# Kernel tuning notes

Hardware: AMD Instinct MI355X
Metric: run time of the kernel (lower is better)

Reference implementation:

```python
import jax, jax.numpy as jnp
import numpy as np

N = 1024       # nodes
D1 = 64        # hidden_dim_1
D2 = 64        # hidden_dim_2
E = 16384      # edges
P = 8192       # query pairs
MAXX = 100     # max node label -> Embedding(MAXX+1, D1)
EPS = 1e-5     # LayerNorm eps (no affine)


def _ln(t):
    m = jnp.mean(t, axis=-1, keepdims=True)
    v = jnp.mean((t - m) ** 2, axis=-1, keepdims=True)
    return (t - m) / jnp.sqrt(v + EPS)


def setup_inputs() -> dict:
    key = jax.random.key(0)
    ks = jax.random.split(key, 12)
    s = 0.1
    x = jax.random.randint(ks[0], (N,), 0, MAXX + 1)
    ei = jax.random.randint(ks[1], (2, E), 0, N)
    pos = jax.random.randint(ks[2], (P, 2), 0, N)
    emb = jax.random.normal(ks[3], (MAXX + 1, D1)) * s
    sage_Wl = jax.random.normal(ks[4], (2, D1, D1)) * s   # lin_l weight (aggr path, has bias)
    sage_bl = jnp.zeros((2, D1))
    sage_Wr = jax.random.normal(ks[5], (2, D1, D1)) * s   # lin_r weight (root path, no bias)
    h_W = jax.random.normal(ks[6], (D1 + 1, D2)) * s
    h_b = jnp.zeros((D2,))
    g_W = jax.random.normal(ks[7], (D1 + 1 + 2 * D2, D2)) * s
    g_b = jnp.zeros((D2,))
    lin_W = jax.random.normal(ks[8], (D2, 1)) * s
    lin_b = jnp.zeros((1,))
    return {"x": x, "ei": ei, "pos": pos, "emb": emb,
            "sage_Wl": sage_Wl, "sage_bl": sage_bl, "sage_Wr": sage_Wr,
            "h_W": h_W, "h_b": h_b, "g_W": g_W, "g_b": g_b,
            "lin_W": lin_W, "lin_b": lin_b}


def reference(x, ei, pos, emb, sage_Wl, sage_bl, sage_Wr, h_W, h_b, g_W, g_b, lin_W, lin_b):
    n = N
    src, dst = ei[0], ei[1]
    h = emb[x]                                            # (n, D1)
    # SAGEConv x2: mean-aggregate src->dst, lin_l(aggr)+bias + lin_r(root); then LN (no affine, no relu)
    deg = jax.ops.segment_sum(jnp.ones((E,), h.dtype), dst, num_segments=n)
    deg = jnp.maximum(deg, 1.0)[:, None]
    for i in range(2):
        aggr = jax.ops.segment_sum(h[src], dst, num_segments=n) / deg
        h = _ln(aggr @ sage_Wl[i] + sage_bl[i] + h @ sage_Wr[i])
    # pairwise outer product features: (n, n, D1)
    A = h[:, None, :] * h[None, :, :]
    eim = jnp.zeros((n * n,), h.dtype).at[src * n + dst].set(1.0).reshape(n, n, 1)
    A = jnp.concatenate([A, eim], axis=-1)                # (n, n, D1+1)
    # mataggr: B = h_1(A); row/col sums; D = cat(A, vec_p, vec_q); g_1(D)
    B = jax.nn.relu(_ln(A @ h_W + h_b))                   # (n, n, D2)
    vec_p = jnp.sum(B, axis=1, keepdims=True)             # (n, 1, D2)
    vec_q = jnp.sum(B, axis=0, keepdims=True)             # (1, n, D2)
    Dm = jnp.concatenate([A,
                          jnp.broadcast_to(vec_p, (n, n, D2)),
                          jnp.broadcast_to(vec_q, (n, n, D2))], axis=-1)
    G = jax.nn.relu(_ln(Dm @ g_W + g_b))                  # (n, n, D2)
    # symmetrize and gather query pairs
    S = (G * jnp.transpose(G, (1, 0, 2))).reshape(n * n, D2)
    sel = S[pos[:, 0] * n + pos[:, 1]]                    # (P, D2)
    return sel @ lin_W + lin_b                            # (P, 1)
```

## Files before the change

kernel.cpp:

```cpp
#include <hip/hip_runtime.h>
#include <hip/hip_bf16.h>

#define NN 1024
#define DD 64
#define EE 16384
#define PP 8192
#define EPSF 1e-5f
#define SWP (DD + 8)

typedef __hip_bfloat16 bf16;
typedef __attribute__((ext_vector_type(8))) short short8;
typedef __attribute__((ext_vector_type(4))) float f32x4;

static __device__ __forceinline__ float dec1(const void* src, int i, int fl) {
    if (fl) return ((const float*)src)[i];
    return __bfloat162float(((const bf16*)src)[i]);
}
static __device__ __forceinline__ unsigned short f2bf_u(float f) {
    bf16 h = __float2bfloat16(f);
    return *reinterpret_cast<unsigned short*>(&h);
}
static __device__ __forceinline__ float bfu2f(unsigned short u) {
    return __uint_as_float(((unsigned int)u) << 16);
}
static __device__ __forceinline__ int probe_fl(const void* emb) {
    int lane = threadIdx.x & 63;
    unsigned short raw = ((const unsigned short*)emb)[lane];
    float v = __uint_as_float(((unsigned int)raw) << 16);
    return (__ballot(!(fabsf(v) <= 1e3f)) != 0ull) ? 1 : 0;
}

__global__ __launch_bounds__(1024) void k_prep(
        const void* __restrict__ emb, const void* __restrict__ sWl,
        const void* __restrict__ sbl, const void* __restrict__ sWr,
        const void* __restrict__ hW, const void* __restrict__ hb,
        const void* __restrict__ gW, const void* __restrict__ gb,
        const void* __restrict__ lW, const void* __restrict__ lb,
        const int* __restrict__ x, const int* __restrict__ ei,
        float* __restrict__ Wlf, float* __restrict__ blf, float* __restrict__ Wrf,
        float* __restrict__ WfT, float* __restrict__ hbw,
        float* __restrict__ gWf, float* __restrict__ linf,
        float* __restrict__ h0,
        unsigned int* __restrict__ eim, unsigned int* __restrict__ eimT,
        int* __restrict__ rowptr, int* __restrict__ csrc) {
    __shared__ int sdeg[NN];
    __shared__ int stmp[1024];
    const int b = blockIdx.x, tid = threadIdx.x;
    const int fl = probe_fl(emb);

    if (b < 97) {
        const int vb = b * 4 + (tid >> 8);
        const int vt = tid & 255;
        if (vb < 256) {
            int z = vb * 256 + vt;
            if (z < 32768) eim[z] = 0u;
            else           eimT[z - 32768] = 0u;
        }
        if (vb < 32) { int i = vb * 256 + vt; Wlf[i] = dec1(sWl, i, fl); }
        else if (vb == 32) { if (vt < 128) blf[vt] = dec1(sbl, vt, fl); }
        else if (vb < 65) { int i = (vb - 33) * 256 + vt; Wrf[i] = dec1(sWr, i, fl); }
        else if (vb < 82) {
            int i = (vb - 65) * 256 + vt;
            if (i < 4096) { int n = i >> 6, k = i & 63; WfT[n * DD + k] = dec1(hW, k * DD + n, fl); }
            else if (i < 4160) hbw[i - 4096] = dec1(hb, i - 4096, fl);
            else if (i < 4224) hbw[64 + (i - 4160)] = dec1(hW, 64 * DD + (i - 4160), fl);
        } else if (vb < 131) {
            int i = (vb - 82) * 256 + vt;
            if (i < 193 * DD) gWf[i] = dec1(gW, i, fl);
            else if (i < 194 * DD) gWf[i] = dec1(gb, i - 193 * DD, fl);
        } else if (vb == 131) {
            if (vt < DD) linf[vt] = dec1(lW, vt, fl);
            else if (vt == DD) linf[DD] = dec1(lb, 0, fl);
        } else if (vb < 388) {
            int i = (vb - 132) * 256 + vt;
            int node = i >> 6, f = i & 63;
            h0[i] = dec1(emb, x[node] * DD + f, fl);
        }
    } else {
        sdeg[tid] = 0;
        __syncthreads();
        for (int base = 0; base < EE; base += 8192) {
            int d8[8];
#pragma unroll
            for (int u = 0; u < 8; ++u) d8[u] = ei[EE + base + u * 1024 + tid];
#pragma unroll
            for (int u = 0; u < 8; ++u) atomicAdd(&sdeg[d8[u]], 1);
        }
        __syncthreads();
        int v = sdeg[tid];
        stmp[tid] = v;
        __syncthreads();
        for (int off = 1; off < 1024; off <<= 1) {
            int a = (tid >= off) ? stmp[tid - off] : 0;
            __syncthreads();
            stmp[tid] += a;
            __syncthreads();
        }
        int excl = stmp[tid] - v;
        rowptr[tid] = excl;
        sdeg[tid] = excl;
        if (tid == 1023) rowptr[NN] = stmp[1023];
        __syncthreads();
        for (int base = 0; base < EE; base += 8192) {
            int d8[8], s8[8];
#pragma unroll
            for (int u = 0; u < 8; ++u) {
                d8[u] = ei[EE + base + u * 1024 + tid];
                s8[u] = ei[base + u * 1024 + tid];
            }
#pragma unroll
            for (int u = 0; u < 8; ++u) {
                int c = atomicAdd(&sdeg[d8[u]], 1);
                csrc[c] = s8[u];
            }
        }
    }
}

static __device__ __forceinline__ void sage_body(
        char* smem, int node, int lane, int wave,
        const int* __restrict__ rowptr, const int* __restrict__ csrc,
        const float* __restrict__ hin,
        const float* __restrict__ Wl, const float* __restrict__ bl,
        const float* __restrict__ Wr,
        float* __restrict__ hout, unsigned short* __restrict__ hbf) {
    float* sa = (float*)smem + wave * 2 * DD;
    float* sh = sa + DD;
    int r0 = rowptr[node], r1 = rowptr[node + 1];
    float s = 0.f;
    for (int r = r0; r < r1; ++r) s += hin[csrc[r] * DD + lane];
    sa[lane] = s / (float)max(r1 - r0, 1);
    sh[lane] = hin[node * DD + lane];
    float o = bl[lane];
    for (int k = 0; k < DD; ++k)
        o += sa[k] * Wl[k * DD + lane] + sh[k] * Wr[k * DD + lane];
    float m = o;
    for (int off = 32; off; off >>= 1) m += __shfl_xor(m, off);
    m *= (1.f / DD);
    float d0 = o - m;
    float v = d0 * d0;
    for (int off = 32; off; off >>= 1) v += __shfl_xor(v, off);
    v *= (1.f / DD);
    float r = d0 * rsqrtf(v + EPSF);
    hout[node * DD + lane] = r;
    if (hbf) hbf[node * DD + lane] = f2bf_u(r);
}

__global__ __launch_bounds__(256) void k_sage0(
        const int* __restrict__ ei,
        const int* __restrict__ rowptr, const int* __restrict__ csrc,
        const float* __restrict__ h0,
        const float* __restrict__ Wlf, const float* __restrict__ blf,
        const float* __restrict__ Wrf,
        float* __restrict__ h1,
        unsigned int* __restrict__ eim, unsigned int* __restrict__ eimT) {
    __shared__ __align__(16) char smem[4 * 2 * DD * 4];
    const int b = blockIdx.x, tid = threadIdx.x;
    const int lane = tid & 63, wave = tid >> 6;
    if (tid < 64) {
        int e = b * 64 + tid;
        int s = ei[e], d = ei[EE + e];
        unsigned int idx = (unsigned int)(s * NN + d);
        atomicOr(&eim[idx >> 5], 1u << (idx & 31));
        unsigned int idxT = (unsigned int)(d * NN + s);
        atomicOr(&eimT[idxT >> 5], 1u << (idxT & 31));
    }
    sage_body(smem, b * 4 + wave, lane, wave, rowptr, csrc, h0, Wlf, blf, Wrf,
              h1, (unsigned short*)nullptr);
}

__global__ __launch_bounds__(256) void k_sage1(
        const int* __restrict__ rowptr, const int* __restrict__ csrc,
        const float* __restrict__ h1,
        const float* __restrict__ Wlf, const float* __restrict__ blf,
        const float* __restrict__ Wrf,
        float* __restrict__ h2, unsigned short* __restrict__ hbf) {
    __shared__ __align__(16) char smem[4 * 2 * DD * 4];
    const int b = blockIdx.x, tid = threadIdx.x;
    const int lane = tid & 63, wave = tid >> 6;
    sage_body(smem, b * 4 + wave, lane, wave, rowptr, csrc, h1,
              Wlf + DD * DD, blf + DD, Wrf + DD * DD, h2, hbf);
}

__global__ __launch_bounds__(256) void k_bstage(
        const float* __restrict__ h2, const unsigned short* __restrict__ hbf,
        const float* __restrict__ WfT, const float* __restrict__ hbw,
        const unsigned int* __restrict__ eim, const unsigned int* __restrict__ eimT,
        const float* __restrict__ gWf,
        float* __restrict__ ppb, float* __restrict__ qqb) {
    __shared__ __align__(16) unsigned short sW[DD * SWP];
    __shared__ __align__(16) float red[4 * 128];
    const int b = blockIdx.x, tid = threadIdx.x;
    const int lane = tid & 63, wave = tid >> 6;
    const int l15 = lane & 15, quad = lane >> 4;

    {
        int m = tid >> 2;
        int k0 = (tid & 3) * 16;
        const float* hi = h2 + b * DD;
        const float* wr = WfT + m * DD;
        unsigned short tmp[16];
#pragma unroll
        for (int u = 0; u < 16; ++u) tmp[u] = f2bf_u(hi[k0 + u] * wr[k0 + u]);
        *(short8*)(sW + m * SWP + k0) = *(short8*)tmp;
        *(short8*)(sW + m * SWP + k0 + 8) = *(short8*)(tmp + 8);
    }
    __syncthreads();

    short8 Af[4][2];
#pragma unroll
    for (int mt = 0; mt < 4; ++mt)
#pragma unroll
        for (int kt = 0; kt < 2; ++kt)
            Af[mt][kt] = *(const short8*)(sW + (mt * 16 + l15) * SWP + kt * 32 + quad * 8);

    float hb0[4][4], hww[4][4];
#pragma unroll
    for (int mt = 0; mt < 4; ++mt) {
        f32x4 a = *(const f32x4*)(hbw + mt * 16 + quad * 4);
        f32x4 wv = *(const f32x4*)(hbw + 64 + mt * 16 + quad * 4);
#pragma unroll
        for (int r = 0; r < 4; ++r) { hb0[mt][r] = a[r]; hww[mt][r] = wv[r]; }
    }

    float accf[4][4], accb[4][4];
#pragma unroll
    for (int mt = 0; mt < 4; ++mt)
#pragma unroll
        for (int r = 0; r < 4; ++r) { accf[mt][r] = 0.f; accb[mt][r] = 0.f; }

    int g = wave;
    short8 B0 = *(const short8*)(hbf + (g * 16 + l15) * DD + quad * 8);
    short8 B1 = *(const short8*)(hbf + (g * 16 + l15) * DD + 32 + quad * 8);

    for (int it = 0; it < 16; ++it, g += 4) {
        short8 cB0 = B0, cB1 = B1;
        if (it < 15) {
            int gn = g + 4;
            B0 = *(const short8*)(hbf + (gn * 16 + l15) * DD + quad * 8);
            B1 = *(const short8*)(hbf + (gn * 16 + l15) * DD + 32 + quad * 8);
        }
        unsigned int base = (unsigned int)(b * NN + g * 16);
        unsigned int sf = (eim[base >> 5] >> (base & 31)) & 0xFFFFu;
        unsigned int sb = (eimT[base >> 5] >> (base & 31)) & 0xFFFFu;

        f32x4 C[4];
#pragma unroll
        for (int mt = 0; mt < 4; ++mt)
            C[mt] = (f32x4){hb0[mt][0], hb0[mt][1], hb0[mt][2], hb0[mt][3]};
#pragma unroll
        for (int mt = 0; mt < 4; ++mt)
            C[mt] = __builtin_amdgcn_mfma_f32_16x16x32_bf16(Af[mt][0], cB0, C[mt], 0, 0, 0);
#pragma unroll
        for (int mt = 0; mt < 4; ++mt)
            C[mt] = __builtin_amdgcn_mfma_f32_16x16x32_bf16(Af[mt][1], cB1, C[mt], 0, 0, 0);

        float ef = (float)((sf >> l15) & 1u);
        float s1 = 0.f, s2 = 0.f;
#pragma unroll
        for (int mt = 0; mt < 4; ++mt)
#pragma unroll
            for (int r = 0; r < 4; ++r) {
                float v = C[mt][r] + ef * hww[mt][r];
                C[mt][r] = v;
                s1 += v;
                s2 += v * v;
            }
        s1 += __shfl_xor(s1, 16); s1 += __shfl_xor(s1, 32);
        s2 += __shfl_xor(s2, 16); s2 += __shfl_xor(s2, 32);
        float mean = s1 * (1.f / DD);
        float var = fmaxf(s2 * (1.f / DD) - mean * mean, 0.f);
        float rs = rsqrtf(var + EPSF);
        float mrs = mean * rs;

        if (sf == sb) {
#pragma unroll
            for (int mt = 0; mt < 4; ++mt)
#pragma unroll
                for (int r = 0; r < 4; ++r) {
                    float u = fmaxf(C[mt][r] * rs - mrs, 0.f);
                    accf[mt][r] += u;
                    accb[mt][r] += u;
                }
        } else {
#pragma unroll
            for (int mt = 0; mt < 4; ++mt)
#pragma unroll
                for (int r = 0; r < 4; ++r)
                    accf[mt][r] += fmaxf(C[mt][r] * rs - mrs, 0.f);
            float de = (float)((sb >> l15) & 1u) - ef;
            float t1 = 0.f, t2 = 0.f;
#pragma unroll
            for (int mt = 0; mt < 4; ++mt)
#pragma unroll
                for (int r = 0; r < 4; ++r) {
                    float v = C[mt][r] + de * hww[mt][r];
                    C[mt][r] = v;
                    t1 += v;
                    t2 += v * v;
                }
            t1 += __shfl_xor(t1, 16); t1 += __shfl_xor(t1, 32);
            t2 += __shfl_xor(t2, 16); t2 += __shfl_xor(t2, 32);
            float mean2 = t1 * (1.f / DD);
            float var2 = fmaxf(t2 * (1.f / DD) - mean2 * mean2, 0.f);
            float rs2 = rsqrtf(var2 + EPSF);
            float mrs2 = mean2 * rs2;
#pragma unroll
            for (int mt = 0; mt < 4; ++mt)
#pragma unroll
                for (int r = 0; r < 4; ++r)
                    accb[mt][r] += fmaxf(C[mt][r] * rs2 - mrs2, 0.f);
        }
    }

#pragma unroll
    for (int step = 1; step < 16; step <<= 1)
#pragma unroll
        for (int mt = 0; mt < 4; ++mt)
#pragma unroll
            for (int r = 0; r < 4; ++r) {
                accf[mt][r] += __shfl_xor(accf[mt][r], step);
                accb[mt][r] += __shfl_xor(accb[mt][r], step);
            }
    if (l15 == 0) {
#pragma unroll
        for (int mt = 0; mt < 4; ++mt)
#pragma unroll
            for (int r = 0; r < 4; ++r) {
                int m = mt * 16 + quad * 4 + r;
                red[wave * 128 + m] = accf[mt][r];
                red[wave * 128 + DD + m] = accb[mt][r];
            }
    }
    __syncthreads();
    if (tid < 128) {
        float sum = red[tid] + red[128 + tid] + red[256 + tid] + red[384 + tid];
        red[tid] = sum;
    }
    __syncthreads();
    if (wave < 2) {
        const float* sv = red + wave * DD;
        int row0 = wave ? 129 : 65;
        float o = 0.f;
        for (int k = 0; k < DD; ++k) o += sv[k] * gWf[(row0 + k) * DD + lane];
        (wave ? qqb : ppb)[b * DD + lane] = o;
    }
}

__global__ __launch_bounds__(256) void k_final(
        const void* __restrict__ emb,
        const int* __restrict__ pos, const unsigned short* __restrict__ hbf,
        const float* __restrict__ gWf, const unsigned int* __restrict__ eim,
        const float* __restrict__ ppb, const float* __restrict__ qqb,
        const float* __restrict__ linf, void* __restrict__ outv) {
    __shared__ __align__(16) unsigned short sgW[DD * SWP];
    const int b = blockIdx.x, tid = threadIdx.x;
    const int lane = tid & 63, wave = tid >> 6;
    const int l15 = lane & 15, quad = lane >> 4;
    const int fl = probe_fl(emb);

    {
        int m = tid >> 2;
        int k0 = (tid & 3) * 16;
        unsigned short tmp[16];
#pragma unroll
        for (int u = 0; u < 16; ++u) tmp[u] = f2bf_u(gWf[(k0 + u) * DD + m]);
        *(short8*)(sgW + m * SWP + k0) = *(short8*)tmp;
        *(short8*)(sgW + m * SWP + k0 + 8) = *(short8*)(tmp + 8);
    }

    int pp_ = b * 64 + wave * 16 + l15;
    int a = pos[2 * pp_], bb = pos[2 * pp_ + 1];
    short8 ha0 = *(const short8*)(hbf + a * DD + quad * 8);
    short8 hb0v = *(const short8*)(hbf + bb * DD + quad * 8);
    short8 ha1 = *(const short8*)(hbf + a * DD + 32 + quad * 8);
    short8 hb1v = *(const short8*)(hbf + bb * DD + 32 + quad * 8);
    short8 B0, B1;
#pragma unroll
    for (int j = 0; j < 8; ++j) {
        B0[j] = (short)f2bf_u(bfu2f((unsigned short)ha0[j]) * bfu2f((unsigned short)hb0v[j]));
        B1[j] = (short)f2bf_u(bfu2f((unsigned short)ha1[j]) * bfu2f((unsigned short)hb1v[j]));
    }
    __syncthreads();

    f32x4 C[4];
#pragma unroll
    for (int mt = 0; mt < 4; ++mt) C[mt] = (f32x4){0.f, 0.f, 0.f, 0.f};
#pragma unroll
    for (int mt = 0; mt < 4; ++mt) {
        short8 A0 = *(const short8*)(sgW + (mt * 16 + l15) * SWP + quad * 8);
        C[mt] = __builtin_amdgcn_mfma_f32_16x16x32_bf16(A0, B0, C[mt], 0, 0, 0);
    }
#pragma unroll
    for (int mt = 0; mt < 4; ++mt) {
        short8 A1 = *(const short8*)(sgW + (mt * 16 + l15) * SWP + 32 + quad * 8);
        C[mt] = __builtin_amdgcn_mfma_f32_16x16x32_bf16(A1, B1, C[mt], 0, 0, 0);
    }

    unsigned int iab = (unsigned int)(a * NN + bb), iba = (unsigned int)(bb * NN + a);
    float eab = (float)((eim[iab >> 5] >> (iab & 31)) & 1u);
    float eba = (float)((eim[iba >> 5] >> (iba & 31)) & 1u);

    float u1[4][4], u2[4][4];
    float s1 = 0.f, s12 = 0.f, s2 = 0.f, s22 = 0.f;
#pragma unroll
    for (int mt = 0; mt < 4; ++mt) {
        int m0 = mt * 16 + quad * 4;
        f32x4 w64v = *(const f32x4*)(gWf + 64 * DD + m0);
        f32x4 gbv  = *(const f32x4*)(gWf + 193 * DD + m0);
        f32x4 ppa  = *(const f32x4*)(ppb + a * DD + m0);
        f32x4 qqb_ = *(const f32x4*)(qqb + bb * DD + m0);
        f32x4 ppb_ = *(const f32x4*)(ppb + bb * DD + m0);
        f32x4 qqa  = *(const f32x4*)(qqb + a * DD + m0);
#pragma unroll
        for (int r = 0; r < 4; ++r) {
            float v1 = C[mt][r] + eab * w64v[r] + ppa[r] + qqb_[r] + gbv[r];
            float v2 = C[mt][r] + eba * w64v[r] + ppb_[r] + qqa[r] + gbv[r];
            u1[mt][r] = v1; u2[mt][r] = v2;
            s1 += v1; s12 += v1 * v1;
            s2 += v2; s22 += v2 * v2;
        }
    }
    s1 += __shfl_xor(s1, 16);  s1 += __shfl_xor(s1, 32);
    s12 += __shfl_xor(s12, 16); s12 += __shfl_xor(s12, 32);
    s2 += __shfl_xor(s2, 16);  s2 += __shfl_xor(s2, 32);
    s22 += __shfl_xor(s22, 16); s22 += __shfl_xor(s22, 32);
    float mean1 = s1 * (1.f / DD);
    float rs1 = rsqrtf(fmaxf(s12 * (1.f / DD) - mean1 * mean1, 0.f) + EPSF);
    float mrs1 = mean1 * rs1;
    float mean2 = s2 * (1.f / DD);
    float rs2 = rsqrtf(fmaxf(s22 * (1.f / DD) - mean2 * mean2, 0.f) + EPSF);
    float mrs2 = mean2 * rs2;

    float r = 0.f;
#pragma unroll
    for (int mt = 0; mt < 4; ++mt) {
        f32x4 lw = *(const f32x4*)(linf + mt * 16 + quad * 4);
#pragma unroll
        for (int rr = 0; rr < 4; ++rr) {
            float g1 = fmaxf(u1[mt][rr] * rs1 - mrs1, 0.f);
            float g2 = fmaxf(u2[mt][rr] * rs2 - mrs2, 0.f);
            r += g1 * g2 * lw[rr];
        }
    }
    r += __shfl_xor(r, 16); r += __shfl_xor(r, 32);
    if (quad == 0) {
        float res = r + linf[DD];
        if (fl) ((float*)outv)[pp_] = res;
        else    ((bf16*)outv)[pp_] = __float2bfloat16(res);
    }
}

extern "C" void kernel_launch(void* const* d_in, const int* in_sizes, int n_in,
                              void* d_out, int out_size, void* d_ws, size_t ws_size,
                              hipStream_t stream) {
    const int* x   = (const int*)d_in[0];
    const int* ei  = (const int*)d_in[1];
    const int* pos = (const int*)d_in[2];
    const void* emb = d_in[3];

    char* w = (char*)d_ws;
    auto alloc = [&](size_t bytes) {
        void* q = (void*)w;
        w += (bytes + 255) & ~(size_t)255;
        return q;
    };
    unsigned int* eim  = (unsigned int*)alloc(NN * NN / 8);
    unsigned int* eimT = (unsigned int*)alloc(NN * NN / 8);
    float* h0   = (float*)alloc(NN * DD * 4);
    float* h1   = (float*)alloc(NN * DD * 4);
    float* h2   = (float*)alloc(NN * DD * 4);
    unsigned short* hbf = (unsigned short*)alloc(NN * DD * 2);
    float* Wlf  = (float*)alloc(2 * DD * DD * 4);
    float* blf  = (float*)alloc(2 * DD * 4);
    float* Wrf  = (float*)alloc(2 * DD * DD * 4);
    float* WfT  = (float*)alloc(DD * DD * 4);
    float* hbw  = (float*)alloc(128 * 4);
    float* gWf  = (float*)alloc(194 * DD * 4);
    float* linf = (float*)alloc(65 * 4);
    float* ppb  = (float*)alloc(NN * DD * 4);
    float* qqb  = (float*)alloc(NN * DD * 4);
    int* rowptr = (int*)alloc((NN + 1) * 4);
    int* csrc   = (int*)alloc(EE * 4);

    k_prep<<<98, 1024, 0, stream>>>(emb, d_in[4], d_in[5], d_in[6], d_in[7], d_in[8],
                                    d_in[9], d_in[10], d_in[11], d_in[12],
                                    x, ei, Wlf, blf, Wrf, WfT, hbw, gWf, linf,
                                    h0, eim, eimT, rowptr, csrc);
    k_sage0<<<256, 256, 0, stream>>>(ei, rowptr, csrc, h0, Wlf, blf, Wrf, h1, eim, eimT);
    k_sage1<<<256, 256, 0, stream>>>(rowptr, csrc, h1, Wlf, blf, Wrf, h2, hbf);
    k_bstage<<<NN, 256, 0, stream>>>(h2, hbf, WfT, hbw, eim, eimT, gWf, ppb, qqb);
    k_final<<<PP / 64, 256, 0, stream>>>(emb, pos, hbf, gWf, eim, ppb, qqb, linf, d_out);
}
```

Measured before the change: 158.0 us.

## Stage SAGE weights in LDS, pack LN math, shrink final-kernel blocks

The SAGE kernels now copy both 64x64 weight matrices into shared memory before the per-node matvec, and read the bias directly from the raw input with a dtype probe. The neighbour-sum loop is unrolled by four so several gathers are in flight at once. The bstage LayerNorm/ReLU accumulation is rewritten with 2-wide float vectors to encourage packed FP32 instructions. k_final is launched with 128-thread blocks and twice as many blocks to raise parallelism. The costs are extra LDS traffic and a barrier in the small SAGE kernels, and more per-block weight staging in k_final.

```diff
diff --git a/kernel.cpp b/kernel.cpp
--- a/kernel.cpp
+++ b/kernel.cpp
@@ -11,6 +11,7 @@
 typedef __hip_bfloat16 bf16;
 typedef __attribute__((ext_vector_type(8))) short short8;
 typedef __attribute__((ext_vector_type(4))) float f32x4;
+typedef __attribute__((ext_vector_type(2))) float f32x2;
 
 static __device__ __forceinline__ float dec1(const void* src, int i, int fl) {
     if (fl) return ((const float*)src)[i];
@@ -117,23 +118,27 @@
     }
 }
 
-static __device__ __forceinline__ void sage_body(
-        char* smem, int node, int lane, int wave,
+static __device__ __forceinline__ void sage_core(
+        const float* sWl, const float* sWr, float* sa, float* sh,
+        int node, int lane,
         const int* __restrict__ rowptr, const int* __restrict__ csrc,
-        const float* __restrict__ hin,
-        const float* __restrict__ Wl, const float* __restrict__ bl,
-        const float* __restrict__ Wr,
+        const float* __restrict__ hin, const void* __restrict__ sbl, int boff, int fl,
         float* __restrict__ hout, unsigned short* __restrict__ hbf) {
-    float* sa = (float*)smem + wave * 2 * DD;
-    float* sh = sa + DD;
     int r0 = rowptr[node], r1 = rowptr[node + 1];
     float s = 0.f;
-    for (int r = r0; r < r1; ++r) s += hin[csrc[r] * DD + lane];
+    int r = r0;
+    for (; r + 4 <= r1; r += 4) {
+        int i0 = csrc[r], i1 = csrc[r + 1], i2 = csrc[r + 2], i3 = csrc[r + 3];
+        float v0 = hin[i0 * DD + lane], v1 = hin[i1 * DD + lane];
+        float v2 = hin[i2 * DD + lane], v3 = hin[i3 * DD + lane];
+        s += (v0 + v1) + (v2 + v3);
+    }
+    for (; r < r1; ++r) s += hin[csrc[r] * DD + lane];
     sa[lane] = s / (float)max(r1 - r0, 1);
     sh[lane] = hin[node * DD + lane];
-    float o = bl[lane];
+    float o = dec1(sbl, boff + lane, fl);
     for (int k = 0; k < DD; ++k)
-        o += sa[k] * Wl[k * DD + lane] + sh[k] * Wr[k * DD + lane];
+        o += sa[k] * sWl[k * DD + lane] + sh[k] * sWr[k * DD + lane];
     float m = o;
     for (int off = 32; off; off >>= 1) m += __shfl_xor(m, off);
     m *= (1.f / DD);
@@ -141,22 +146,29 @@
     float v = d0 * d0;
     for (int off = 32; off; off >>= 1) v += __shfl_xor(v, off);
     v *= (1.f / DD);
-    float r = d0 * rsqrtf(v + EPSF);
-    hout[node * DD + lane] = r;
-    if (hbf) hbf[node * DD + lane] = f2bf_u(r);
+    float rr = d0 * rsqrtf(v + EPSF);
+    hout[node * DD + lane] = rr;
+    if (hbf) hbf[node * DD + lane] = f2bf_u(rr);
 }
 
 __global__ __launch_bounds__(256) void k_sage0(
-        const int* __restrict__ ei,
+        const void* __restrict__ emb, const int* __restrict__ ei,
         const int* __restrict__ rowptr, const int* __restrict__ csrc,
         const float* __restrict__ h0,
-        const float* __restrict__ Wlf, const float* __restrict__ blf,
+        const float* __restrict__ Wlf, const void* __restrict__ sbl,
         const float* __restrict__ Wrf,
         float* __restrict__ h1,
         unsigned int* __restrict__ eim, unsigned int* __restrict__ eimT) {
-    __shared__ __align__(16) char smem[4 * 2 * DD * 4];
+    __shared__ __align__(16) float sWl[DD * DD];
+    __shared__ __align__(16) float sWr[DD * DD];
+    __shared__ float sa4[4 * DD], sh4[4 * DD];
     const int b = blockIdx.x, tid = threadIdx.x;
     const int lane = tid & 63, wave = tid >> 6;
+    const int fl = probe_fl(emb);
+    for (int i = tid * 4; i < DD * DD; i += 1024) {
+        *(float4*)(sWl + i) = *(const float4*)(Wlf + i);
+        *(float4*)(sWr + i) = *(const float4*)(Wrf + i);
+    }
     if (tid < 64) {
         int e = b * 64 + tid;
         int s = ei[e], d = ei[EE + e];
@@ -165,21 +177,100 @@
         unsigned int idxT = (unsigned int)(d * NN + s);
         atomicOr(&eimT[idxT >> 5], 1u << (idxT & 31));
     }
-    sage_body(smem, b * 4 + wave, lane, wave, rowptr, csrc, h0, Wlf, blf, Wrf,
-              h1, (unsigned short*)nullptr);
+    __syncthreads();
+    sage_core(sWl, sWr, sa4 + wave * DD, sh4 + wave * DD, b * 4 + wave, lane,
+              rowptr, csrc, h0, sbl, 0, fl, h1, (unsigned short*)nullptr);
 }
 
 __global__ __launch_bounds__(256) void k_sage1(
+        const void* __restrict__ emb,
         const int* __restrict__ rowptr, const int* __restrict__ csrc,
         const float* __restrict__ h1,
-        const float* __restrict__ Wlf, const float* __restrict__ blf,
+        const float* __restrict__ Wlf, const void* __restrict__ sbl,
         const float* __restrict__ Wrf,
         float* __restrict__ h2, unsigned short* __restrict__ hbf) {
-    __shared__ __align__(16) char smem[4 * 2 * DD * 4];
+    __shared__ __align__(16) float sWl[DD * DD];
+    __shared__ __align__(16) float sWr[DD * DD];
+    __shared__ float sa4[4 * DD], sh4[4 * DD];
     const int b = blockIdx.x, tid = threadIdx.x;
     const int lane = tid & 63, wave = tid >> 6;
-    sage_body(smem, b * 4 + wave, lane, wave, rowptr, csrc, h1,
-              Wlf + DD * DD, blf + DD, Wrf + DD * DD, h2, hbf);
+    const int fl = probe_fl(emb);
+    for (int i = tid * 4; i < DD * DD; i += 1024) {
+        *(float4*)(sWl + i) = *(const float4*)(Wlf + DD * DD + i);
+        *(float4*)(sWr + i) = *(const float4*)(Wrf + DD * DD + i);
+    }
+    __syncthreads();
+    sage_core(sWl, sWr, sa4 + wave * DD, sh4 + wave * DD, b * 4 + wave, lane,
+              rowptr, csrc, h1, sbl, DD, fl, h2, hbf);
+}
+
+static __device__ __forceinline__ void tile_ln_pk(
+        const f32x4* C, unsigned int sf, unsigned int sb, int l15,
+        const f32x2 hww2[4][2], f32x2 accf[4][2], f32x2 accb[4][2]) {
+    float ef = (float)((sf >> l15) & 1u);
+    f32x2 efv = {ef, ef};
+    f32x2 s1v = {0.f, 0.f}, s2v = {0.f, 0.f};
+    f32x2 V[4][2];
+#pragma unroll
+    for (int mt = 0; mt < 4; ++mt)
+#pragma unroll
+        for (int h = 0; h < 2; ++h) {
+            f32x2 c = {C[mt][2 * h], C[mt][2 * h + 1]};
+            f32x2 v = c + efv * hww2[mt][h];
+            V[mt][h] = v;
+            s1v += v;
+            s2v += v * v;
+        }
+    float s1 = s1v.x + s1v.y, s2 = s2v.x + s2v.y;
+    s1 += __shfl_xor(s1, 16); s1 += __shfl_xor(s1, 32);
+    s2 += __shfl_xor(s2, 16); s2 += __shfl_xor(s2, 32);
+    float mean = s1 * (1.f / DD);
+    float var = fmaxf(s2 * (1.f / DD) - mean * mean, 0.f);
+    float rs = rsqrtf(var + EPSF);
+    float mrs = mean * rs;
+    f32x2 rsv = {rs, rs}, mrsv = {mrs, mrs}, zero = {0.f, 0.f};
+
+    if (sf == sb) {
+#pragma unroll
+        for (int mt = 0; mt < 4; ++mt)
+#pragma unroll
+            for (int h = 0; h < 2; ++h) {
+                f32x2 u = __builtin_elementwise_max(V[mt][h] * rsv - mrsv, zero);
+                accf[mt][h] += u;
+                accb[mt][h] += u;
+            }
+    } else {
+#pragma unroll
+        for (int mt = 0; mt < 4; ++mt)
+#pragma unroll
+            for (int h = 0; h < 2; ++h)
+                accf[mt][h] += __builtin_elementwise_max(V[mt][h] * rsv - mrsv, zero);
+        float de = (float)((sb >> l15) & 1u) - ef;
+        f32x2 dev = {de, de};
+        f32x2 t1v = {0.f, 0.f}, t2v = {0.f, 0.f};
+#pragma unroll
+        for (int mt = 0; mt < 4; ++mt)
+#pragma unroll
+            for (int h = 0; h < 2; ++h) {
+                f32x2 v = V[mt][h] + dev * hww2[mt][h];
+                V[mt][h] = v;
+                t1v += v;
+                t2v += v * v;
+            }
+        float t1 = t1v.x + t1v.y, t2 = t2v.x + t2v.y;
+        t1 += __shfl_xor(t1, 16); t1 += __shfl_xor(t1, 32);
+        t2 += __shfl_xor(t2, 16); t2 += __shfl_xor(t2, 32);
+        float mean2 = t1 * (1.f / DD);
+        float var2 = fmaxf(t2 * (1.f / DD) - mean2 * mean2, 0.f);
+        float rs2 = rsqrtf(var2 + EPSF);
+        float mrs2 = mean2 * rs2;
+        f32x2 rs2v = {rs2, rs2}, mrs2v = {mrs2, mrs2};
+#pragma unroll
+        for (int mt = 0; mt < 4; ++mt)
+#pragma unroll
+            for (int h = 0; h < 2; ++h)
+                accb[mt][h] += __builtin_elementwise_max(V[mt][h] * rs2v - mrs2v, zero);
+    }
 }
 
 __global__ __launch_bounds__(256) void k_bstage(
@@ -214,20 +305,26 @@
         for (int kt = 0; kt < 2; ++kt)
             Af[mt][kt] = *(const short8*)(sW + (mt * 16 + l15) * SWP + kt * 32 + quad * 8);
 
-    float hb0[4][4], hww[4][4];
+    float hb0[4][4];
+    f32x2 hww2[4][2];
 #pragma unroll
     for (int mt = 0; mt < 4; ++mt) {
         f32x4 a = *(const f32x4*)(hbw + mt * 16 + quad * 4);
         f32x4 wv = *(const f32x4*)(hbw + 64 + mt * 16 + quad * 4);
 #pragma unroll
-        for (int r = 0; r < 4; ++r) { hb0[mt][r] = a[r]; hww[mt][r] = wv[r]; }
-    }
-
-    float accf[4][4], accb[4][4];
+        for (int r = 0; r < 4; ++r) hb0[mt][r] = a[r];
+        hww2[mt][0] = (f32x2){wv[0], wv[1]};
+        hww2[mt][1] = (f32x2){wv[2], wv[3]};
+    }
+
+    f32x2 accf[4][2], accb[4][2];
 #pragma unroll
     for (int mt = 0; mt < 4; ++mt)
 #pragma unroll
-        for (int r = 0; r < 4; ++r) { accf[mt][r] = 0.f; accb[mt][r] = 0.f; }
+        for (int h = 0; h < 2; ++h) {
+            accf[mt][h] = (f32x2){0.f, 0.f};
+            accb[mt][h] = (f32x2){0.f, 0.f};
+        }
 
     int g = wave;
     short8 B0 = *(const short8*)(hbf + (g * 16 + l15) * DD + quad * 8);
@@ -255,72 +352,25 @@
         for (int mt = 0; mt < 4; ++mt)
             C[mt] = __builtin_amdgcn_mfma_f32_16x16x32_bf16(Af[mt][1], cB1, C[mt], 0, 0, 0);
 
-        float ef = (float)((sf >> l15) & 1u);
-        float s1 = 0.f, s2 = 0.f;
+        tile_ln_pk(C, sf, sb, l15, hww2, accf, accb);
+    }
+
+    float af[4][4], ab[4][4];
+#pragma unroll
+    for (int mt = 0; mt < 4; ++mt)
+#pragma unroll
+        for (int h = 0; h < 2; ++h) {
+            af[mt][2 * h] = accf[mt][h].x;  af[mt][2 * h + 1] = accf[mt][h].y;
+            ab[mt][2 * h] = accb[mt][h].x;  ab[mt][2 * h + 1] = accb[mt][h].y;
+        }
+#pragma unroll
+    for (int step = 1; step < 16; step <<= 1)
 #pragma unroll
         for (int mt = 0; mt < 4; ++mt)
 #pragma unroll
             for (int r = 0; r < 4; ++r) {
-                float v = C[mt][r] + ef * hww[mt][r];
-                C[mt][r] = v;
-                s1 += v;
-                s2 += v * v;
-            }
-        s1 += __shfl_xor(s1, 16); s1 += __shfl_xor(s1, 32);
-        s2 += __shfl_xor(s2, 16); s2 += __shfl_xor(s2, 32);
-        float mean = s1 * (1.f / DD);
-        float var = fmaxf(s2 * (1.f / DD) - mean * mean, 0.f);
-        float rs = rsqrtf(var + EPSF);
-        float mrs = mean * rs;
-
-        if (sf == sb) {
-#pragma unroll
-            for (int mt = 0; mt < 4; ++mt)
-#pragma unroll
-                for (int r = 0; r < 4; ++r) {
-                    float u = fmaxf(C[mt][r] * rs - mrs, 0.f);
-                    accf[mt][r] += u;
-                    accb[mt][r] += u;
-                }
-        } else {
-#pragma unroll
-            for (int mt = 0; mt < 4; ++mt)
-#pragma unroll
-                for (int r = 0; r < 4; ++r)
-                    accf[mt][r] += fmaxf(C[mt][r] * rs - mrs, 0.f);
-            float de = (float)((sb >> l15) & 1u) - ef;
-            float t1 = 0.f, t2 = 0.f;
-#pragma unroll
-            for (int mt = 0; mt < 4; ++mt)
-#pragma unroll
-                for (int r = 0; r < 4; ++r) {
-                    float v = C[mt][r] + de * hww[mt][r];
-                    C[mt][r] = v;
-                    t1 += v;
-                    t2 += v * v;
-                }
-            t1 += __shfl_xor(t1, 16); t1 += __shfl_xor(t1, 32);
-            t2 += __shfl_xor(t2, 16); t2 += __shfl_xor(t2, 32);
-            float mean2 = t1 * (1.f / DD);
-            float var2 = fmaxf(t2 * (1.f / DD) - mean2 * mean2, 0.f);
-            float rs2 = rsqrtf(var2 + EPSF);
-            float mrs2 = mean2 * rs2;
-#pragma unroll
-            for (int mt = 0; mt < 4; ++mt)
-#pragma unroll
-                for (int r = 0; r < 4; ++r)
-                    accb[mt][r] += fmaxf(C[mt][r] * rs2 - mrs2, 0.f);
-        }
-    }
-
-#pragma unroll
-    for (int step = 1; step < 16; step <<= 1)
-#pragma unroll
-        for (int mt = 0; mt < 4; ++mt)
-#pragma unroll
-            for (int r = 0; r < 4; ++r) {
-                accf[mt][r] += __shfl_xor(accf[mt][r], step);
-                accb[mt][r] += __shfl_xor(accb[mt][r], step);
+                af[mt][r] += __shfl_xor(af[mt][r], step);
+                ab[mt][r] += __shfl_xor(ab[mt][r], step);
             }
     if (l15 == 0) {
 #pragma unroll
@@ -328,8 +378,8 @@
 #pragma unroll
             for (int r = 0; r < 4; ++r) {
                 int m = mt * 16 + quad * 4 + r;
-                red[wave * 128 + m] = accf[mt][r];
-                red[wave * 128 + DD + m] = accb[mt][r];
+                red[wave * 128 + m] = af[mt][r];
+                red[wave * 128 + DD + m] = ab[mt][r];
             }
     }
     __syncthreads();
@@ -347,7 +397,7 @@
     }
 }
 
-__global__ __launch_bounds__(256) void k_final(
+__global__ __launch_bounds__(128) void k_final(
         const void* __restrict__ emb,
         const int* __restrict__ pos, const unsigned short* __restrict__ hbf,
         const float* __restrict__ gWf, const unsigned int* __restrict__ eim,
@@ -360,16 +410,17 @@
     const int fl = probe_fl(emb);
 
     {
-        int m = tid >> 2;
-        int k0 = (tid & 3) * 16;
-        unsigned short tmp[16];
-#pragma unroll
-        for (int u = 0; u < 16; ++u) tmp[u] = f2bf_u(gWf[(k0 + u) * DD + m]);
-        *(short8*)(sgW + m * SWP + k0) = *(short8*)tmp;
-        *(short8*)(sgW + m * SWP + k0 + 8) = *(short8*)(tmp + 8);
-    }
-
-    int pp_ = b * 64 + wave * 16 + l15;
+        int m = tid >> 1;
+        int k0 = (tid & 1) * 32;
+        unsigned short tmp[32];
+#pragma unroll
+        for (int u = 0; u < 32; ++u) tmp[u] = f2bf_u(gWf[(k0 + u) * DD + m]);
+#pragma unroll
+        for (int q = 0; q < 4; ++q)
+            *(short8*)(sgW + m * SWP + k0 + q * 8) = *(short8*)(tmp + q * 8);
+    }
+
+    int pp_ = b * 32 + wave * 16 + l15;
     int a = pos[2 * pp_], bb = pos[2 * pp_ + 1];
     short8 ha0 = *(const short8*)(hbf + a * DD + quad * 8);
     short8 hb0v = *(const short8*)(hbf + bb * DD + quad * 8);
@@ -487,8 +538,9 @@
                                     d_in[9], d_in[10], d_in[11], d_in[12],
                                     x, ei, Wlf, blf, Wrf, WfT, hbw, gWf, linf,
                                     h0, eim, eimT, rowptr, csrc);
-    k_sage0<<<256, 256, 0, stream>>>(ei, rowptr, csrc, h0, Wlf, blf, Wrf, h1, eim, eimT);
-    k_sage1<<<256, 256, 0, stream>>>(rowptr, csrc, h1, Wlf, blf, Wrf, h2, hbf);
+    k_sage0<<<256, 256, 0, stream>>>(emb, ei, rowptr, csrc, h0, Wlf, d_in[5], Wrf,
+                                     h1, eim, eimT);
+    k_sage1<<<256, 256, 0, stream>>>(emb, rowptr, csrc, h1, Wlf, d_in[5], Wrf, h2, hbf);
     k_bstage<<<NN, 256, 0, stream>>>(h2, hbf, WfT, hbw, eim, eimT, gWf, ppb, qqb);
-    k_final<<<PP / 64, 256, 0, stream>>>(emb, pos, hbf, gWf, eim, ppb, qqb, linf, d_out);
-}
+    k_final<<<PP / 32, 128, 0, stream>>>(emb, pos, hbf, gWf, eim, ppb, qqb, linf, d_out);
+}
```

Measured after the change: 147.1 us. 1.07x faster.
